# Performance work log

Hardware: AMD Instinct MI355X
Metric: run time of the kernel (lower is better)

## Reference

```python
import jax, jax.numpy as jnp
import numpy as np
import math

L_LAYERS = 2; B = 2; SEQ = 1024; D = 512; N = 16; H = 8; DH = 64; P = 32; KC = 4; DTR = 32

def _silu(x):
    return x * jax.nn.sigmoid(x)

def _rms(x, w, eps=1e-6):
    return x * jax.lax.rsqrt(jnp.mean(x * x, axis=-1, keepdims=True) + eps) * w

def _mamba(x, Win, conv_w, conv_b, Wx, Wdt, bdt, Alog, Dp, Wout):
    # x: [b,l,d]; mamba-ssm reference math with expand=1 (d_inner == d)
    b, l, d = x.shape
    xz = x @ Win                                   # [b,l,2d]
    xc, z = jnp.split(xz, 2, axis=-1)
    xp = jnp.pad(xc, ((0, 0), (KC - 1, 0), (0, 0)))  # causal depthwise conv
    xc = sum(xp[:, k:k + l, :] * conv_w[:, k] for k in range(KC)) + conv_b
    xc = _silu(xc)
    dbl = xc @ Wx                                  # [b,l,dtr+2N]
    dt = dbl[..., :DTR]
    Bc = dbl[..., DTR:DTR + N]                     # [b,l,N]
    Cc = dbl[..., DTR + N:]                        # [b,l,N]
    dt = jax.nn.softplus(dt @ Wdt + bdt)           # [b,l,d]
    A = -jnp.exp(Alog)                             # [d,N]
    dA = jnp.exp(dt[..., None] * A)                # [b,l,d,N]
    dBu = dt[..., None] * Bc[:, :, None, :] * xc[..., None]  # [b,l,d,N]
    def step(h, inp):
        dA_t, dBu_t, C_t = inp
        h = dA_t * h + dBu_t                       # [b,d,N]
        return h, jnp.einsum('bdn,bn->bd', h, C_t)
    h0 = jnp.zeros((b, d, N), x.dtype)
    _, ys = jax.lax.scan(step, h0, (dA.transpose(1, 0, 2, 3), dBu.transpose(1, 0, 2, 3), Cc.transpose(1, 0, 2)))
    y = ys.transpose(1, 0, 2) + Dp * xc
    y = y * _silu(z)
    return y @ Wout

def _enformer_attn(q, k, vv, u, vb, w):
    # q,k,vv: [b,l,h,d]; u,vb: [h,d]; w: [h,d,P]
    b, l, h, d = q.shape
    Pd = w.shape[-1]
    pos = jnp.arange(l)
    dist = pos[None, :] - pos[:, None]             # [l,l]
    pow_rate = jnp.exp(jnp.log((l + 1) / 2.0) / (Pd // 2))
    cw = pow_rate ** jnp.arange(1, Pd // 2 + 1, dtype=jnp.float32)
    ub = (jnp.abs(dist)[:, :, None].astype(jnp.float32) <= cw)
    sb = jnp.sign(dist)[:, :, None].astype(jnp.float32) * ub.astype(jnp.float32)
    basis = jnp.concatenate([ub.astype(jnp.float32), sb], axis=-1)  # [l,l,P]
    scale = 1.0 / math.sqrt(d)
    # qr_term without materializing r[h,l,l,d]: (q@w) then contract with basis
    qw = jnp.einsum('bihd,hdn->bhin', q, w)
    qr = jnp.einsum('bhin,ijn->bhij', qw, basis)
    uk = jnp.einsum('hd,bjhd->bhj', u, k)[:, :, None, :]
    vr = jnp.einsum('hn,ijn->hij', jnp.einsum('hd,hdn->hn', vb, w), basis)
    scores = jnp.einsum('bihd,bjhd->bhij', q, k) * scale + (qr + uk + vr[None]) * scale
    attn = jax.nn.softmax(scores, axis=-1)
    return jnp.einsum('bhij,bjhd->bihd', attn, vv)

def _forward(x, rms_m, W_in, b_in, m_Win, m_conv_w, m_conv_b, m_Wx, m_Wdt, m_bdt, m_Alog, m_D, m_Wout, W_out, b_out, rms_a, Wq, Wk, Wv, u, v, w_rel, Wo, b_o):
    b, l, dm = x.shape
    for i in range(L_LAYERS):
        # --- BidirectionalMamba block (tie_in_proj=True, tie_gate=False) ---
        skip = x
        xn = _rms(x, rms_m[i])
        proj = xn @ W_in[i] + b_in[i]              # [b,l,3*dm]
        xf = proj[..., :dm]
        zf = proj[..., dm:2 * dm]
        zr = proj[..., 2 * dm:]
        yf = _mamba(xf, m_Win[i, 0], m_conv_w[i, 0], m_conv_b[i, 0], m_Wx[i, 0], m_Wdt[i, 0], m_bdt[i, 0], m_Alog[i, 0], m_D[i, 0], m_Wout[i, 0])
        yr = jnp.flip(_mamba(jnp.flip(xf, axis=1), m_Win[i, 1], m_conv_w[i, 1], m_conv_b[i, 1], m_Wx[i, 1], m_Wdt[i, 1], m_bdt[i, 1], m_Alog[i, 1], m_D[i, 1], m_Wout[i, 1]), axis=1)
        y = yf * _silu(zf) + yr * _silu(zr)
        x = y @ W_out[i] + b_out[i] + skip
        # --- Enformer relative-position attention block ---
        skip = x
        xn = _rms(x, rms_a[i])
        q = (xn @ Wq[i]).reshape(b, l, H, DH)
        k = (xn @ Wk[i]).reshape(b, l, H, DH)
        vv = (xn @ Wv[i]).reshape(b, l, H, DH)
        o = _enformer_attn(q, k, vv, u[i], v[i], w_rel[i]).reshape(b, l, H * DH)
        x = skip + o @ Wo[i] + b_o[i]
    return x

def setup_inputs() -> dict:
    key = jax.random.key(0)
    ks = iter(jax.random.split(key, 48))
    def rn(shape, s=0.02):
        return jax.random.normal(next(ks), shape, dtype=jnp.float32) * s
    L = L_LAYERS
    inp = {}
    inp['x'] = jax.random.normal(next(ks), (B, SEQ, D), dtype=jnp.float32)
    inp['rms_m'] = jnp.ones((L, D), jnp.float32)
    inp['W_in'] = rn((L, D, 3 * D)); inp['b_in'] = jnp.zeros((L, 3 * D), jnp.float32)
    inp['m_Win'] = rn((L, 2, D, 2 * D))
    inp['m_conv_w'] = rn((L, 2, D, KC), 0.1); inp['m_conv_b'] = jnp.zeros((L, 2, D), jnp.float32)
    inp['m_Wx'] = rn((L, 2, D, DTR + 2 * N))
    inp['m_Wdt'] = rn((L, 2, DTR, D), 0.1); inp['m_bdt'] = rn((L, 2, D), 0.5)
    inp['m_Alog'] = jnp.tile(jnp.log(jnp.arange(1, N + 1, dtype=jnp.float32)), (L, 2, D, 1))
    inp['m_D'] = jnp.ones((L, 2, D), jnp.float32)
    inp['m_Wout'] = rn((L, 2, D, D))
    inp['W_out'] = rn((L, D, D)); inp['b_out'] = jnp.zeros((L, D), jnp.float32)
    inp['rms_a'] = jnp.ones((L, D), jnp.float32)
    inp['Wq'] = rn((L, D, H * DH)); inp['Wk'] = rn((L, D, H * DH)); inp['Wv'] = rn((L, D, H * DH))
    inp['u'] = rn((L, H, DH), 0.1); inp['v'] = rn((L, H, DH), 0.1)
    inp['w_rel'] = rn((L, H, DH, P), 0.1)
    inp['Wo'] = rn((L, H * DH, D)); inp['b_o'] = jnp.zeros((L, D), jnp.float32)
    return inp

def reference(x, rms_m, W_in, b_in, m_Win, m_conv_w, m_conv_b, m_Wx, m_Wdt, m_bdt, m_Alog, m_D, m_Wout, W_out, b_out, rms_a, Wq, Wk, Wv, u, v, w_rel, Wo, b_o):
    return _forward(x, rms_m, W_in, b_in, m_Win, m_conv_w, m_conv_b, m_Wx, m_Wdt, m_bdt, m_Alog, m_D, m_Wout, W_out, b_out, rms_a, Wq, Wk, Wv, u, v, w_rel, Wo, b_o)
```

## Files before the change

### kernel.cpp

```cpp
#include <hip/hip_runtime.h>

#define LL 2
#define BB 2
#define SEQL 1024
#define DD 512
#define NN 16
#define HH 8
#define DHH 64
#define PPB 32
#define KCC 4
#define DTRR 32

#define GBS 4
#define TC 32
#define NC (SEQL / TC)
#define NR (GBS * DD * NN)
#define BHN (BB * HH * SEQL)

#define AR_L     4325376L
#define OFF_WIN  0L
#define OFF_MWIN 786432L
#define OFF_WT2  1835008L
#define OFF_MWOUT 2490368L
#define OFF_WOUT 3014656L
#define OFF_QKV  3276800L
#define OFF_WO   4063232L

typedef __attribute__((ext_vector_type(8))) short bf16x8;
typedef __attribute__((ext_vector_type(4))) short short4v;
typedef __attribute__((ext_vector_type(4))) float f32x4;

__device__ __forceinline__ float siluf(float x) { return x / (1.f + __expf(-x)); }
__device__ __forceinline__ float softplusf(float x) { return x > 20.f ? x : log1pf(__expf(x)); }

__device__ __forceinline__ unsigned short f2bf(float x) {
  union { float f; unsigned u; } v; v.f = x;
  unsigned r = v.u + 0x7fff + ((v.u >> 16) & 1);
  return (unsigned short)(r >> 16);
}

__device__ __forceinline__ bf16x8 ld_frag(const unsigned short* p) {
  short4v a = *(const short4v*)(p);
  short4v b = *(const short4v*)(p + 4);
  bf16x8 r;
  r[0]=a[0]; r[1]=a[1]; r[2]=a[2]; r[3]=a[3];
  r[4]=b[0]; r[5]=b[1]; r[6]=b[2]; r[7]=b[3];
  return r;
}

__device__ __forceinline__ bf16x8 pack8(const float* p) {
  bf16x8 r;
  #pragma unroll
  for (int e = 0; e < 8; e++) r[e] = (short)f2bf(p[e]);
  return r;
}

struct TD { const float* src; unsigned short* dst; int ldsrc; int K; int N; int t0; };
struct TDs { TD a[24]; };

__global__ __launch_bounds__(256) void wtrans_all(TDs ds)
{
  int bid = blockIdx.x;
  int mi = 0;
  #pragma unroll 1
  for (int i = 1; i < 24; i++) if (bid >= ds.a[i].t0) mi = i;
  TD d = ds.a[mi];
  int local = bid - d.t0;
  int tilesN = d.N >> 5;
  int tn = local % tilesN, tk = local / tilesN;
  __shared__ float t[32][33];
  int tx = threadIdx.x & 31, ty = threadIdx.x >> 5;
  int n0 = tn * 32, k0 = tk * 32;
  #pragma unroll
  for (int i = 0; i < 4; i++)
    t[ty + 8 * i][tx] = d.src[(long)(k0 + ty + 8 * i) * d.ldsrc + n0 + tx];
  __syncthreads();
  #pragma unroll
  for (int i = 0; i < 4; i++)
    d.dst[(long)(n0 + ty + 8 * i) * d.K + k0 + tx] = f2bf(t[tx][ty + 8 * i]);
}

__global__ __launch_bounds__(256) void weff_kernel(
    const float* __restrict__ Wx, const float* __restrict__ Wdt,
    unsigned short* __restrict__ WTA)
{
  int lg = blockIdx.z;
  int l = lg >> 1, g = lg & 1;
  const float* wx = Wx + (long)(l * 2 + g) * DD * 64;
  const float* wd = Wdt + (long)(l * 2 + g) * DTRR * DD;
  unsigned short* wt = WTA + (long)l * AR_L + OFF_WT2 + (long)g * 327680;
  int n0 = blockIdx.x * 32, k0 = blockIdx.y * 32;
  __shared__ float wx_s[32][33];
  __shared__ float wd_s[32][33];
  int tx = threadIdx.x & 31, ty = threadIdx.x >> 5;
  #pragma unroll
  for (int i = 0; i < 4; i++) {
    wx_s[ty + 8 * i][tx] = wx[(long)(k0 + ty + 8 * i) * 64 + tx];
    wd_s[ty + 8 * i][tx] = wd[(long)(ty + 8 * i) * DD + n0 + tx];
  }
  __syncthreads();
  #pragma unroll
  for (int i = 0; i < 4; i++) {
    int nl = ty + 8 * i;
    float s = 0.f;
    #pragma unroll
    for (int r = 0; r < 32; r++) s = fmaf(wx_s[tx][r], wd_s[r][nl], s);
    wt[(long)(n0 + nl) * DD + k0 + tx] = f2bf(s);
  }
}

__global__ __launch_bounds__(256) void rmsinv_kernel(
    const float* __restrict__ x, float* __restrict__ inv)
{
  int row = blockIdx.x * 4 + (threadIdx.x >> 6);
  int lane = threadIdx.x & 63;
  const float* xr = x + (long)row * DD;
  float4 a = *(const float4*)(xr + lane * 4);
  float4 b = *(const float4*)(xr + 256 + lane * 4);
  float s = a.x*a.x + a.y*a.y + a.z*a.z + a.w*a.w + b.x*b.x + b.y*b.y + b.z*b.z + b.w*b.w;
  for (int o = 32; o; o >>= 1) s += __shfl_down(s, o);
  if (lane == 0) inv[row] = rsqrtf(s / (float)DD + 1e-6f);
}

template<int BM, int BN>
__global__ __launch_bounds__(256) void gemm_bf16_t(
    const float* __restrict__ A, const unsigned short* __restrict__ WT,
    const float* __restrict__ bias, const float* __restrict__ resid,
    const float* __restrict__ invrow, const float* __restrict__ colw,
    float* __restrict__ C,
    int M, int N, int K, int lda, int ldc,
    long aBatch, long wBatch, long biasBatch, long cBatch,
    int aflipL, int act)
{
  constexpr int FM = BM / 32;
  constexpr int FN = BN / 32;
  int g = blockIdx.z;
  A  += (long)g * aBatch;
  WT += (long)g * wBatch;
  C  += (long)g * cBatch;
  if (bias) bias += (long)g * biasBatch;
  const bool flip = (aflipL > 0) && (g == 1);

  __shared__ unsigned short A_lds[BM][72];
  __shared__ unsigned short B_lds[BN][72];
  int tid = threadIdx.x;
  int w = tid >> 6, lane = tid & 63, li = lane & 15, lg = lane >> 4;
  int bm = blockIdx.y * BM, bn = blockIdx.x * BN;
  int wm = (w & 1) * (BM / 2), wn = (w >> 1) * (BN / 2);
  f32x4 acc[FM][FN] = {};

  const int kqA = (tid & 15) * 4, r0A = tid >> 4;
  const int kqB = (tid & 7) * 8,  r0B = tid >> 3;

  for (int k0 = 0; k0 < K; k0 += 64) {
    __syncthreads();
    float4 cw4 = {1.f, 1.f, 1.f, 1.f};
    if (colw) cw4 = *(const float4*)(colw + k0 + kqA);
    #pragma unroll
    for (int i = 0; i < BM / 16; i++) {
      int m = bm + r0A + 16 * i;
      int mm = m;
      if (flip) { int bb = m / aflipL; int t = m - bb * aflipL; mm = bb * aflipL + (aflipL - 1 - t); }
      float4 av = *(const float4*)(A + (long)mm * lda + k0 + kqA);
      float sc = invrow ? invrow[mm] : 1.f;
      short4v ap = { (short)f2bf(av.x * sc * cw4.x), (short)f2bf(av.y * sc * cw4.y),
                     (short)f2bf(av.z * sc * cw4.z), (short)f2bf(av.w * sc * cw4.w) };
      *(short4v*)(&A_lds[r0A + 16 * i][kqA]) = ap;
    }
    #pragma unroll
    for (int i = 0; i < BN / 32; i++) {
      int n = bn + r0B + 32 * i;
      bf16x8 bv = *(const bf16x8*)(WT + (long)n * K + k0 + kqB);
      *(bf16x8*)(&B_lds[r0B + 32 * i][kqB]) = bv;
    }
    __syncthreads();
    #pragma unroll
    for (int ks = 0; ks < 2; ks++) {
      bf16x8 af[FM], bfr[FN];
      #pragma unroll
      for (int fm = 0; fm < FM; fm++)
        af[fm] = *(const bf16x8*)(&A_lds[wm + fm * 16 + li][ks * 32 + lg * 8]);
      #pragma unroll
      for (int fn = 0; fn < FN; fn++)
        bfr[fn] = *(const bf16x8*)(&B_lds[wn + fn * 16 + li][ks * 32 + lg * 8]);
      #pragma unroll
      for (int fm = 0; fm < FM; fm++)
        #pragma unroll
        for (int fn = 0; fn < FN; fn++)
          acc[fm][fn] = __builtin_amdgcn_mfma_f32_16x16x32_bf16(af[fm], bfr[fn], acc[fm][fn], 0, 0, 0);
    }
  }
  #pragma unroll
  for (int fm = 0; fm < FM; fm++) {
    #pragma unroll
    for (int fn = 0; fn < FN; fn++) {
      int n = bn + wn + fn * 16 + li;
      float bv = bias ? bias[n] : 0.f;
      #pragma unroll
      for (int r = 0; r < 4; r++) {
        int m = bm + wm + fm * 16 + 4 * lg + r;
        float v = acc[fm][fn][r] + bv;
        if (act == 1) v = softplusf(v);
        if (resid) v += resid[(long)m * ldc + n];
        C[(long)m * ldc + n] = v;
      }
    }
  }
}

__global__ __launch_bounds__(256) void gemm_comb(
    const float* __restrict__ yp, const float* __restrict__ proj,
    const unsigned short* __restrict__ WT,
    const float* __restrict__ bias, const float* __restrict__ resid,
    float* __restrict__ C)
{
  __shared__ unsigned short A_lds[64][72];
  __shared__ unsigned short B_lds[64][72];
  int tid = threadIdx.x;
  int w = tid >> 6, lane = tid & 63, li = lane & 15, lg = lane >> 4;
  int bm = blockIdx.y * 64, bn = blockIdx.x * 64;
  int wm = (w & 1) * 32, wn = (w >> 1) * 32;
  f32x4 acc[2][2] = {};
  const long U = (long)BB * SEQL * DD;

  const int kqA = (tid & 15) * 4, r0A = tid >> 4;
  const int kqB = (tid & 7) * 8,  r0B = tid >> 3;

  for (int k0 = 0; k0 < DD; k0 += 64) {
    __syncthreads();
    #pragma unroll
    for (int i = 0; i < 4; i++) {
      int m = bm + r0A + 16 * i;
      int t = m & (SEQL - 1), b = m >> 10;
      int mf = (b << 10) + (SEQL - 1 - t);
      float4 y0 = *(const float4*)(yp + (long)m * DD + k0 + kqA);
      float4 y1 = *(const float4*)(yp + U + (long)mf * DD + k0 + kqA);
      float4 zf = *(const float4*)(proj + (long)m * 3 * DD + DD + k0 + kqA);
      float4 zr = *(const float4*)(proj + (long)m * 3 * DD + 2 * DD + k0 + kqA);
      float4 v;
      v.x = y0.x * siluf(zf.x) + y1.x * siluf(zr.x);
      v.y = y0.y * siluf(zf.y) + y1.y * siluf(zr.y);
      v.z = y0.z * siluf(zf.z) + y1.z * siluf(zr.z);
      v.w = y0.w * siluf(zf.w) + y1.w * siluf(zr.w);
      short4v ap = { (short)f2bf(v.x), (short)f2bf(v.y), (short)f2bf(v.z), (short)f2bf(v.w) };
      *(short4v*)(&A_lds[r0A + 16 * i][kqA]) = ap;
    }
    #pragma unroll
    for (int i = 0; i < 2; i++) {
      int n = bn + r0B + 32 * i;
      bf16x8 bv = *(const bf16x8*)(WT + (long)n * DD + k0 + kqB);
      *(bf16x8*)(&B_lds[r0B + 32 * i][kqB]) = bv;
    }
    __syncthreads();
    #pragma unroll
    for (int ks = 0; ks < 2; ks++) {
      bf16x8 af[2], bfr[2];
      #pragma unroll
      for (int fm = 0; fm < 2; fm++)
        af[fm] = *(const bf16x8*)(&A_lds[wm + fm * 16 + li][ks * 32 + lg * 8]);
      #pragma unroll
      for (int fn = 0; fn < 2; fn++)
        bfr[fn] = *(const bf16x8*)(&B_lds[wn + fn * 16 + li][ks * 32 + lg * 8]);
      #pragma unroll
      for (int fm = 0; fm < 2; fm++)
        #pragma unroll
        for (int fn = 0; fn < 2; fn++)
          acc[fm][fn] = __builtin_amdgcn_mfma_f32_16x16x32_bf16(af[fm], bfr[fn], acc[fm][fn], 0, 0, 0);
    }
  }
  #pragma unroll
  for (int fm = 0; fm < 2; fm++) {
    #pragma unroll
    for (int fn = 0; fn < 2; fn++) {
      int n = bn + wn + fn * 16 + li;
      float bv = bias[n];
      #pragma unroll
      for (int r = 0; r < 4; r++) {
        int m = bm + wm + fm * 16 + 4 * lg + r;
        C[(long)m * DD + n] = acc[fm][fn][r] + bv + resid[(long)m * DD + n];
      }
    }
  }
}

__global__ __launch_bounds__(256) void gemm_attn(
    const float* __restrict__ opart, const float* __restrict__ mbuf, const float* __restrict__ lbuf,
    const unsigned short* __restrict__ WT,
    const float* __restrict__ bias, const float* __restrict__ resid,
    float* __restrict__ C)
{
  __shared__ unsigned short A_lds[64][72];
  __shared__ unsigned short B_lds[64][72];
  int tid = threadIdx.x;
  int w = tid >> 6, lane = tid & 63, li = lane & 15, lg = lane >> 4;
  int bm = blockIdx.y * 64, bn = blockIdx.x * 64;
  int wm = (w & 1) * 32, wn = (w >> 1) * 32;
  f32x4 acc[2][2] = {};

  const int kqA = (tid & 15) * 4, r0A = tid >> 4;
  const int kqB = (tid & 7) * 8,  r0B = tid >> 3;

  for (int k0 = 0; k0 < DD; k0 += 64) {
    __syncthreads();
    int h = k0 >> 6;
    #pragma unroll
    for (int i = 0; i < 4; i++) {
      int m = bm + r0A + 16 * i;
      int iseq = m & (SEQL - 1), b = m >> 10;
      long row = ((long)(b * HH + h) << 10) + iseq;
      float m0 = mbuf[row], m1 = mbuf[BHN + row];
      float l0 = lbuf[row], l1 = lbuf[BHN + row];
      float mm = fmaxf(m0, m1);
      float e0 = __expf(m0 - mm), e1 = __expf(m1 - mm);
      float inv = 1.f / (l0 * e0 + l1 * e1);
      e0 *= inv; e1 *= inv;
      float4 o0 = *(const float4*)(opart + row * 64 + kqA);
      float4 o1 = *(const float4*)(opart + ((long)BHN + row) * 64 + kqA);
      float4 v;
      v.x = o0.x * e0 + o1.x * e1;
      v.y = o0.y * e0 + o1.y * e1;
      v.z = o0.z * e0 + o1.z * e1;
      v.w = o0.w * e0 + o1.w * e1;
      short4v ap = { (short)f2bf(v.x), (short)f2bf(v.y), (short)f2bf(v.z), (short)f2bf(v.w) };
      *(short4v*)(&A_lds[r0A + 16 * i][kqA]) = ap;
    }
    #pragma unroll
    for (int i = 0; i < 2; i++) {
      int n = bn + r0B + 32 * i;
      bf16x8 bv = *(const bf16x8*)(WT + (long)n * DD + k0 + kqB);
      *(bf16x8*)(&B_lds[r0B + 32 * i][kqB]) = bv;
    }
    __syncthreads();
    #pragma unroll
    for (int ks = 0; ks < 2; ks++) {
      bf16x8 af[2], bfr[2];
      #pragma unroll
      for (int fm = 0; fm < 2; fm++)
        af[fm] = *(const bf16x8*)(&A_lds[wm + fm * 16 + li][ks * 32 + lg * 8]);
      #pragma unroll
      for (int fn = 0; fn < 2; fn++)
        bfr[fn] = *(const bf16x8*)(&B_lds[wn + fn * 16 + li][ks * 32 + lg * 8]);
      #pragma unroll
      for (int fm = 0; fm < 2; fm++)
        #pragma unroll
        for (int fn = 0; fn < 2; fn++)
          acc[fm][fn] = __builtin_amdgcn_mfma_f32_16x16x32_bf16(af[fm], bfr[fn], acc[fm][fn], 0, 0, 0);
    }
  }
  #pragma unroll
  for (int fm = 0; fm < 2; fm++) {
    #pragma unroll
    for (int fn = 0; fn < 2; fn++) {
      int n = bn + wn + fn * 16 + li;
      float bv = bias[n];
      #pragma unroll
      for (int r = 0; r < 4; r++) {
        int m = bm + wm + fm * 16 + 4 * lg + r;
        C[(long)m * DD + n] = acc[fm][fn][r] + bv + resid[(long)m * DD + n];
      }
    }
  }
}

__global__ __launch_bounds__(256) void gemm_dtbc(
    const float* __restrict__ A, const unsigned short* __restrict__ WT2,
    const float* __restrict__ bdt, float* __restrict__ dtv, float* __restrict__ bc,
    int layer)
{
  int g = blockIdx.z;
  A   += (long)g * BB * SEQL * DD;
  WT2 += (long)g * 640 * DD;
  dtv += (long)g * BB * SEQL * DD;
  bc  += (long)g * BB * SEQL * 32;
  bdt += (long)(layer * 2 + g) * DD;

  __shared__ unsigned short A_lds[64][72];
  __shared__ unsigned short B_lds[64][72];
  int tid = threadIdx.x;
  int w = tid >> 6, lane = tid & 63, li = lane & 15, lg = lane >> 4;
  int bm = blockIdx.y * 64, bn = blockIdx.x * 64;
  int wm = (w & 1) * 32, wn = (w >> 1) * 32;
  f32x4 acc[2][2] = {};

  const int kqA = (tid & 15) * 4, r0A = tid >> 4;
  const int kqB = (tid & 7) * 8,  r0B = tid >> 3;

  for (int k0 = 0; k0 < DD; k0 += 64) {
    __syncthreads();
    #pragma unroll
    for (int i = 0; i < 4; i++) {
      int m = bm + r0A + 16 * i;
      float4 av = *(const float4*)(A + (long)m * DD + k0 + kqA);
      short4v ap = { (short)f2bf(av.x), (short)f2bf(av.y), (short)f2bf(av.z), (short)f2bf(av.w) };
      *(short4v*)(&A_lds[r0A + 16 * i][kqA]) = ap;
    }
    #pragma unroll
    for (int i = 0; i < 2; i++) {
      int n = bn + r0B + 32 * i;
      bf16x8 bv = *(const bf16x8*)(WT2 + (long)n * DD + k0 + kqB);
      *(bf16x8*)(&B_lds[r0B + 32 * i][kqB]) = bv;
    }
    __syncthreads();
    #pragma unroll
    for (int ks = 0; ks < 2; ks++) {
      bf16x8 af[2], bfr[2];
      #pragma unroll
      for (int fm = 0; fm < 2; fm++)
        af[fm] = *(const bf16x8*)(&A_lds[wm + fm * 16 + li][ks * 32 + lg * 8]);
      #pragma unroll
      for (int fn = 0; fn < 2; fn++)
        bfr[fn] = *(const bf16x8*)(&B_lds[wn + fn * 16 + li][ks * 32 + lg * 8]);
      #pragma unroll
      for (int fm = 0; fm < 2; fm++)
        #pragma unroll
        for (int fn = 0; fn < 2; fn++)
          acc[fm][fn] = __builtin_amdgcn_mfma_f32_16x16x32_bf16(af[fm], bfr[fn], acc[fm][fn], 0, 0, 0);
    }
  }
  #pragma unroll
  for (int fm = 0; fm < 2; fm++) {
    #pragma unroll
    for (int fn = 0; fn < 2; fn++) {
      int n = bn + wn + fn * 16 + li;
      if (n < 512) {
        float bv = bdt[n];
        #pragma unroll
        for (int r = 0; r < 4; r++) {
          int m = bm + wm + fm * 16 + 4 * lg + r;
          dtv[(long)m * DD + n] = softplusf(acc[fm][fn][r] + bv);
        }
      } else if (n < 544) {
        #pragma unroll
        for (int r = 0; r < 4; r++) {
          int m = bm + wm + fm * 16 + 4 * lg + r;
          bc[(long)m * 32 + (n - 512)] = acc[fm][fn][r];
        }
      }
    }
  }
}

__global__ __launch_bounds__(256) void conv_silu_kernel(
    const float* __restrict__ xz, const float* __restrict__ cw, const float* __restrict__ cb,
    float* __restrict__ xc, int layer)
{
  long idx = (long)blockIdx.x * 256 + threadIdx.x;
  int c = idx % DD;
  long r = idx / DD;
  int t = r % SEQL;
  long gb = r / SEQL;
  int g = (int)(gb / BB);
  const float* w = cw + ((long)(layer * 2 + g) * DD + c) * KCC;
  float acc = cb[(long)(layer * 2 + g) * DD + c];
  const float* xp = xz + (r - t) * 2 * DD + c;
  #pragma unroll
  for (int k = 0; k < KCC; k++) {
    int tt = t - (KCC - 1) + k;
    if (tt >= 0) acc = fmaf(xp[(long)tt * 2 * DD], w[k], acc);
  }
  xc[idx] = siluf(acc);
}

__global__ __launch_bounds__(256) void scan_chunk_kernel(
    const float* __restrict__ dtv, const float* __restrict__ xc,
    const float* __restrict__ bc, const float* __restrict__ Alog,
    float* __restrict__ P, float* __restrict__ Hend, int layer)
{
  int chunk = blockIdx.x, dtile = blockIdx.y, gb = blockIdx.z;
  int g = gb / BB;
  int tid = threadIdx.x;
  int dl = tid >> 1, nh = (tid & 1) * 8;
  int d = dtile * 128 + dl;
  int t0 = chunk * TC;
  __shared__ float dtv_s[TC][128], xc_s[TC][128], BC_s[TC][32];
  {
    long base = ((long)gb * SEQL + t0) * DD + dtile * 128;
    int c4 = (tid & 31) * 4, r0 = tid >> 5;
    #pragma unroll
    for (int i = 0; i < 4; i++) {
      int tl = r0 + i * 8;
      *(float4*)&dtv_s[tl][c4] = *(const float4*)(dtv + base + (long)tl * DD + c4);
      *(float4*)&xc_s[tl][c4]  = *(const float4*)(xc + base + (long)tl * DD + c4);
    }
    long dbase = ((long)gb * SEQL + t0) * 32;
    int cc = (tid & 7) * 4, rr = tid >> 3;
    *(float4*)&BC_s[rr][cc] = *(const float4*)(bc + dbase + (long)rr * 32 + cc);
  }
  __syncthreads();
  const float* Al = Alog + ((long)((layer * 2 + g) * DD) + d) * NN + nh;
  float a[8], h[8] = {};
  #pragma unroll
  for (int n = 0; n < 8; n++) a[n] = -__expf(Al[n]);
  float sdt = 0.f;
  for (int t = 0; t < TC; t++) {
    float dt = dtv_s[t][dl];
    float dx = dt * xc_s[t][dl];
    float4 b0 = *(const float4*)&BC_s[t][nh];
    float4 b1 = *(const float4*)&BC_s[t][nh + 4];
    h[0] = fmaf(__expf(dt * a[0]), h[0], dx * b0.x);
    h[1] = fmaf(__expf(dt * a[1]), h[1], dx * b0.y);
    h[2] = fmaf(__expf(dt * a[2]), h[2], dx * b0.z);
    h[3] = fmaf(__expf(dt * a[3]), h[3], dx * b0.w);
    h[4] = fmaf(__expf(dt * a[4]), h[4], dx * b1.x);
    h[5] = fmaf(__expf(dt * a[5]), h[5], dx * b1.y);
    h[6] = fmaf(__expf(dt * a[6]), h[6], dx * b1.z);
    h[7] = fmaf(__expf(dt * a[7]), h[7], dx * b1.w);
    sdt += dt;
  }
  long o = (long)chunk * NR + ((long)(gb * DD + d)) * NN + nh;
  #pragma unroll
  for (int n = 0; n < 8; n++) {
    P[o + n] = __expf(a[n] * sdt);
    Hend[o + n] = h[n];
  }
}

__global__ __launch_bounds__(256) void scan_combine_kernel(
    const float* __restrict__ P, const float* __restrict__ Hend, float* __restrict__ Hin)
{
  int r = blockIdx.x * 256 + threadIdx.x;
  float h = 0.f;
  #pragma unroll
  for (int c = 0; c < NC; c++) {
    Hin[(long)c * NR + r] = h;
    h = fmaf(P[(long)c * NR + r], h, Hend[(long)c * NR + r]);
  }
}

__global__ __launch_bounds__(256) void scan_apply_kernel(
    const float* __restrict__ dtv, const float* __restrict__ xc, const float* __restrict__ xz,
    const float* __restrict__ bc, const float* __restrict__ Alog, const float* __restrict__ Dp,
    const float* __restrict__ Hin, float* __restrict__ ym, int layer)
{
  int chunk = blockIdx.x, dtile = blockIdx.y, gb = blockIdx.z;
  int g = gb / BB;
  int tid = threadIdx.x;
  int dl = tid >> 1, nh = (tid & 1) * 8;
  int d = dtile * 128 + dl;
  int t0 = chunk * TC;
  __shared__ float dtv_s[TC][128], xc_s[TC][128], BC_s[TC][32], y_s[TC][128];
  {
    long base = ((long)gb * SEQL + t0) * DD + dtile * 128;
    int c4 = (tid & 31) * 4, r0 = tid >> 5;
    #pragma unroll
    for (int i = 0; i < 4; i++) {
      int tl = r0 + i * 8;
      *(float4*)&dtv_s[tl][c4] = *(const float4*)(dtv + base + (long)tl * DD + c4);
      *(float4*)&xc_s[tl][c4]  = *(const float4*)(xc + base + (long)tl * DD + c4);
    }
    long dbase = ((long)gb * SEQL + t0) * 32;
    int cc = (tid & 7) * 4, rr = tid >> 3;
    *(float4*)&BC_s[rr][cc] = *(const float4*)(bc + dbase + (long)rr * 32 + cc);
  }
  __syncthreads();
  const float* Al = Alog + ((long)((layer * 2 + g) * DD) + d) * NN + nh;
  float a[8], h[8];
  #pragma unroll
  for (int n = 0; n < 8; n++) a[n] = -__expf(Al[n]);
  {
    long r = (long)chunk * NR + ((long)(gb * DD + d)) * NN + nh;
    float4 h0 = *(const float4*)(Hin + r);
    float4 h1 = *(const float4*)(Hin + r + 4);
    h[0]=h0.x; h[1]=h0.y; h[2]=h0.z; h[3]=h0.w;
    h[4]=h1.x; h[5]=h1.y; h[6]=h1.z; h[7]=h1.w;
  }
  for (int t = 0; t < TC; t++) {
    float dt = dtv_s[t][dl];
    float dx = dt * xc_s[t][dl];
    float4 b0 = *(const float4*)&BC_s[t][nh];
    float4 b1 = *(const float4*)&BC_s[t][nh + 4];
    float4 c0 = *(const float4*)&BC_s[t][16 + nh];
    float4 c1 = *(const float4*)&BC_s[t][16 + nh + 4];
    h[0] = fmaf(__expf(dt * a[0]), h[0], dx * b0.x);
    h[1] = fmaf(__expf(dt * a[1]), h[1], dx * b0.y);
    h[2] = fmaf(__expf(dt * a[2]), h[2], dx * b0.z);
    h[3] = fmaf(__expf(dt * a[3]), h[3], dx * b0.w);
    h[4] = fmaf(__expf(dt * a[4]), h[4], dx * b1.x);
    h[5] = fmaf(__expf(dt * a[5]), h[5], dx * b1.y);
    h[6] = fmaf(__expf(dt * a[6]), h[6], dx * b1.z);
    h[7] = fmaf(__expf(dt * a[7]), h[7], dx * b1.w);
    float v0 = h[0] * c0.x + h[1] * c0.y;
    float v1 = h[2] * c0.z + h[3] * c0.w;
    float v2 = h[4] * c1.x + h[5] * c1.y;
    float v3 = h[6] * c1.z + h[7] * c1.w;
    float val = (v0 + v1) + (v2 + v3);
    val += __shfl_xor(val, 1);
    if ((tid & 1) == 0) y_s[t][dl] = val;
  }
  __syncthreads();
  {
    long base = ((long)gb * SEQL + t0) * DD + dtile * 128;
    long zbase = ((long)gb * SEQL + t0) * 2 * DD + DD + dtile * 128;
    int c4 = (tid & 31) * 4, r0 = tid >> 5;
    float4 Dp4 = *(const float4*)(Dp + (long)(layer * 2 + g) * DD + dtile * 128 + c4);
    #pragma unroll
    for (int i = 0; i < 4; i++) {
      int tl = r0 + i * 8;
      float4 y4 = *(const float4*)&y_s[tl][c4];
      float4 x4 = *(const float4*)&xc_s[tl][c4];
      float4 z4 = *(const float4*)(xz + zbase + (long)tl * 2 * DD + c4);
      float4 o;
      o.x = (y4.x + Dp4.x * x4.x) * siluf(z4.x);
      o.y = (y4.y + Dp4.y * x4.y) * siluf(z4.y);
      o.z = (y4.z + Dp4.z * x4.z) * siluf(z4.z);
      o.w = (y4.w + Dp4.w * x4.w) * siluf(z4.w);
      *(float4*)(ym + base + (long)tl * DD + c4) = o;
    }
  }
}

__global__ void tab_kernel(unsigned short* __restrict__ tab)
{
  int idx = blockIdx.x * blockDim.x + threadIdx.x;
  if (idx >= 2047) return;
  int di = idx - 1023;
  int ad = di < 0 ? -di : di;
  float pr = expf(logf((SEQL + 1) * 0.5f) / 16.0f);
  int n0 = 16;
  for (int n = 15; n >= 0; n--) {
    float cw = powf(pr, (float)(n + 1));
    if ((float)ad <= cw) n0 = n;
  }
  tab[idx] = (unsigned short)(di == 0 ? 34 : (di < 0 ? n0 : 17 + n0));
}

__global__ __launch_bounds__(256) void qw_kernel(
    const float* __restrict__ q, const float* __restrict__ w_rel, float* __restrict__ S, int layer)
{
  int itile = blockIdx.x;
  int bh = blockIdx.y;
  int h = bh % HH, b = bh / HH;
  int i0 = itile * 64;
  __shared__ float q_s[64][65];
  __shared__ float w_s[64][33];
  __shared__ float qwn[64][33];
  int tid = threadIdx.x;
  {
    int r = tid >> 2, c4 = (tid & 3) * 16;
    const float* qr = q + ((long)(b * SEQL + i0 + r)) * DD + h * 64 + c4;
    #pragma unroll
    for (int e = 0; e < 4; e++) {
      float4 v = *(const float4*)(qr + e * 4);
      q_s[r][c4 + e * 4 + 0] = v.x; q_s[r][c4 + e * 4 + 1] = v.y;
      q_s[r][c4 + e * 4 + 2] = v.z; q_s[r][c4 + e * 4 + 3] = v.w;
    }
  }
  for (int idx = tid; idx < 64 * 32; idx += 256) {
    int d = idx >> 5, n = idx & 31;
    w_s[d][n] = w_rel[((long)(layer * HH + h) * DHH + d) * PPB + n];
  }
  __syncthreads();
  {
    int i = tid & 63, ngrp = tid >> 6;
    float acc[8] = {};
    #pragma unroll 8
    for (int d = 0; d < 64; d++) {
      float qv = q_s[i][d];
      #pragma unroll
      for (int e = 0; e < 8; e++) acc[e] = fmaf(qv, w_s[d][ngrp * 8 + e], acc[e]);
    }
    #pragma unroll
    for (int e = 0; e < 8; e++) qwn[i][ngrp * 8 + e] = acc[e];
  }
  __syncthreads();
  for (int idx = tid; idx < 64 * 17; idx += 256) {
    int il = idx / 17, m = idx % 17;
    float s1 = 0.f, s2 = 0.f;
    for (int n = m; n < 16; n++) { s1 += qwn[il][n]; s2 += qwn[il][16 + n]; }
    float* Sp = S + ((long)bh * SEQL + i0 + il) * 34;
    Sp[m] = s1;
    Sp[17 + m] = s2;
  }
}

__global__ __launch_bounds__(256) void vw_kernel(
    const float* __restrict__ vparam, const float* __restrict__ w_rel, float* __restrict__ VS)
{
  int layer = blockIdx.x;
  __shared__ float vws[HH][PPB];
  int tid = threadIdx.x;
  int h = tid / PPB, n = tid % PPB;
  const float* vp = vparam + (long)(layer * HH + h) * DHH;
  const float* wp = w_rel + ((long)(layer * HH + h) * DHH) * PPB + n;
  float s = 0.f;
  for (int d = 0; d < DHH; d++) s = fmaf(vp[d], wp[d * PPB], s);
  vws[h][n] = s;
  __syncthreads();
  if (tid < HH * 17) {
    int hh = tid / 17, m = tid % 17;
    float s1 = 0.f, s2 = 0.f;
    for (int nn = m; nn < 16; nn++) { s1 += vws[hh][nn]; s2 += vws[hh][16 + nn]; }
    VS[layer * 272 + hh * 34 + m] = s1;
    VS[layer * 272 + hh * 34 + 17 + m] = s2;
  }
}

__global__ __launch_bounds__(256) void uk_kernel(
    const float* __restrict__ u, const float* __restrict__ k, float* __restrict__ uk, int layer)
{
  int wid = (blockIdx.x * 256 + threadIdx.x) >> 6;
  int lane = threadIdx.x & 63;
  if (wid >= BB * HH * SEQL) return;
  int j = wid % SEQL;
  int bh = wid / SEQL;
  int h = bh % HH;
  int b = bh / HH;
  float vv = u[(long)(layer * HH + h) * DHH + lane] * k[((long)(b * SEQL + j) * HH + h) * DHH + lane];
  for (int o = 32; o; o >>= 1) vv += __shfl_down(vv, o);
  if (lane == 0) uk[(long)bh * SEQL + j] = vv;
}

__global__ __launch_bounds__(256) void attn_mfma_kernel(
    const float* __restrict__ q, const float* __restrict__ k, const float* __restrict__ vv,
    const float* __restrict__ S, const float* __restrict__ VS, const float* __restrict__ uk,
    const unsigned short* __restrict__ tab,
    float* __restrict__ opart, float* __restrict__ mbuf, float* __restrict__ lbuf)
{
  __shared__ __align__(16) char smem[39680];
  unsigned short* K_lds  = (unsigned short*)(smem);
  unsigned short* VT_lds = (unsigned short*)(smem + 8704);
  unsigned short* PT_lds = (unsigned short*)(smem + 17408);
  float* E               = (float*)(smem + 26112);
  unsigned short* tab_s  = (unsigned short*)(smem + 35328);
  float* uk_s            = (float*)(smem + 39424);
  float* O_lds           = (float*)(smem);

  int itile = blockIdx.x;
  int bh = blockIdx.y;
  int split = blockIdx.z;
  int h = bh % HH, b = bh / HH;
  int i0 = itile * 64;
  int tid = threadIdx.x;
  int w = tid >> 6;
  int lane = tid & 63;
  int li = lane & 15, lg = lane >> 4;

  for (int idx = tid; idx < 64 * 17; idx += 256) {
    int il = idx / 17, m = idx % 17;
    long srow = ((long)bh * SEQL + i0 + il) * 34;
    float c0 = S[srow + m]      + VS[h * 34 + m];
    float c1 = S[srow + 17 + m] + VS[h * 34 + 17 + m];
    E[il * 36 + m]      = c0 - c1;
    E[il * 36 + 17 + m] = c0 + c1;
    if (m == 0) E[il * 36 + 34] = c0;
  }
  for (int idx = tid; idx < 2047; idx += 256) tab_s[idx] = tab[idx];

  int iq = i0 + w * 16 + li;
  const float* qrow = q + ((long)(b * SEQL + iq)) * DD + h * 64;
  bf16x8 qf0 = pack8(qrow + 8 * lg);
  bf16x8 qf1 = pack8(qrow + 32 + 8 * lg);

  f32x4 oacc[4] = {};
  float mrun = -1e30f, lrun = 0.f;
  const int ibase = i0 + w * 16 + li;
  unsigned short* PTw = PT_lds + w * 16 * 68;
  const float* Erow = E + (w * 16 + li) * 36;

  const int jbase = split * (SEQL / 2);
  for (int jt = 0; jt < SEQL / 2; jt += 64) {
    int j0 = jbase + jt;
    __syncthreads();
    {
      int jl = tid >> 4;
      int dq = (tid & 15) * 4;
      #pragma unroll
      for (int rr = 0; rr < 4; rr++) {
        int jj = jl + rr * 16;
        long grow = ((long)(b * SEQL + j0 + jj)) * DD + h * 64 + dq;
        float4 kv = *(const float4*)(k + grow);
        short4v kp = { (short)f2bf(kv.x), (short)f2bf(kv.y), (short)f2bf(kv.z), (short)f2bf(kv.w) };
        *(short4v*)(K_lds + jj * 68 + dq) = kp;
        float4 vvv = *(const float4*)(vv + grow);
        VT_lds[(dq + 0) * 68 + jj] = f2bf(vvv.x);
        VT_lds[(dq + 1) * 68 + jj] = f2bf(vvv.y);
        VT_lds[(dq + 2) * 68 + jj] = f2bf(vvv.z);
        VT_lds[(dq + 3) * 68 + jj] = f2bf(vvv.w);
      }
      if (tid < 64) uk_s[tid] = uk[(long)bh * SEQL + j0 + tid];
    }
    __syncthreads();

    f32x4 sf[4];
    #pragma unroll
    for (int jj = 0; jj < 4; jj++) {
      f32x4 c = {};
      c = __builtin_amdgcn_mfma_f32_16x16x32_bf16(
            ld_frag(K_lds + (jj * 16 + li) * 68 + 8 * lg), qf0, c, 0, 0, 0);
      c = __builtin_amdgcn_mfma_f32_16x16x32_bf16(
            ld_frag(K_lds + (jj * 16 + li) * 68 + 32 + 8 * lg), qf1, c, 0, 0, 0);
      sf[jj] = c;
    }

    float sv[4][4];
    float tmax = -1e30f;
    #pragma unroll
    for (int jj = 0; jj < 4; jj++) {
      #pragma unroll
      for (int r = 0; r < 4; r++) {
        int jloc = jj * 16 + 4 * lg + r;
        int di = (j0 + jloc) - ibase;
        int id = tab_s[1023 + di];
        float val = (sf[jj][r] + Erow[id] + uk_s[jloc]) * 0.125f;
        sv[jj][r] = val;
        tmax = fmaxf(tmax, val);
      }
    }
    tmax = fmaxf(tmax, __shfl_xor(tmax, 16));
    tmax = fmaxf(tmax, __shfl_xor(tmax, 32));
    float mnew = fmaxf(mrun, tmax);
    float fsc = __expf(mrun - mnew);
    mrun = mnew;
    lrun *= fsc;
    #pragma unroll
    for (int df = 0; df < 4; df++) oacc[df] *= fsc;

    float psum = 0.f;
    #pragma unroll
    for (int jj = 0; jj < 4; jj++) {
      short4v pk;
      #pragma unroll
      for (int r = 0; r < 4; r++) {
        float p = __expf(sv[jj][r] - mnew);
        psum += p;
        pk[r] = (short)f2bf(p);
      }
      *(short4v*)(PTw + li * 68 + jj * 16 + 4 * lg) = pk;
    }
    psum += __shfl_xor(psum, 16);
    psum += __shfl_xor(psum, 32);
    lrun += psum;

    asm volatile("s_waitcnt lgkmcnt(0)" ::: "memory");

    bf16x8 pf0 = ld_frag(PTw + li * 68 + 8 * lg);
    bf16x8 pf1 = ld_frag(PTw + li * 68 + 32 + 8 * lg);
    #pragma unroll
    for (int df = 0; df < 4; df++) {
      f32x4 c = oacc[df];
      c = __builtin_amdgcn_mfma_f32_16x16x32_bf16(
            ld_frag(VT_lds + (df * 16 + li) * 68 + 8 * lg), pf0, c, 0, 0, 0);
      c = __builtin_amdgcn_mfma_f32_16x16x32_bf16(
            ld_frag(VT_lds + (df * 16 + li) * 68 + 32 + 8 * lg), pf1, c, 0, 0, 0);
      oacc[df] = c;
    }
  }

  __syncthreads();
  if (lg == 0) {
    long row = (long)split * BHN + (long)bh * SEQL + (i0 + w * 16 + li);
    mbuf[row] = mrun;
    lbuf[row] = lrun;
  }
  #pragma unroll
  for (int df = 0; df < 4; df++)
    *(f32x4*)(O_lds + (w * 16 + li) * 68 + df * 16 + 4 * lg) = oacc[df];
  __syncthreads();
  {
    int il = tid >> 2, c0 = (tid & 3) * 16;
    long orow = ((long)split * BHN + (long)bh * SEQL + i0 + il) * 64 + c0;
    #pragma unroll
    for (int c4 = 0; c4 < 4; c4++) {
      f32x4 o = *(const f32x4*)(O_lds + il * 68 + c0 + c4 * 4);
      *(f32x4*)(opart + orow + c4 * 4) = o;
    }
  }
}

extern "C" void kernel_launch(void* const* d_in, const int* in_sizes, int n_in,
                              void* d_out, int out_size, void* d_ws, size_t ws_size,
                              hipStream_t stream) {
  const float* x_in     = (const float*)d_in[0];
  const float* rms_m    = (const float*)d_in[1];
  const float* W_in     = (const float*)d_in[2];
  const float* b_in     = (const float*)d_in[3];
  const float* m_Win    = (const float*)d_in[4];
  const float* m_conv_w = (const float*)d_in[5];
  const float* m_conv_b = (const float*)d_in[6];
  const float* m_Wx     = (const float*)d_in[7];
  const float* m_Wdt    = (const float*)d_in[8];
  const float* m_bdt    = (const float*)d_in[9];
  const float* m_Alog   = (const float*)d_in[10];
  const float* m_Dp     = (const float*)d_in[11];
  const float* m_Wout   = (const float*)d_in[12];
  const float* W_out    = (const float*)d_in[13];
  const float* b_out    = (const float*)d_in[14];
  const float* rms_a    = (const float*)d_in[15];
  const float* Wq       = (const float*)d_in[16];
  const float* Wk       = (const float*)d_in[17];
  const float* Wv       = (const float*)d_in[18];
  const float* u_p      = (const float*)d_in[19];
  const float* v_p      = (const float*)d_in[20];
  const float* w_rel    = (const float*)d_in[21];
  const float* Wo       = (const float*)d_in[22];
  const float* b_o      = (const float*)d_in[23];
  float* out = (float*)d_out;

  float* ws = (float*)d_ws;
  const long U = (long)BB * SEQL * DD;
  float* xA    = ws;
  float* xB    = ws + 1 * U;
  float* xn    = ws + 2 * U;
  float* proj  = ws + 3 * U;
  float* xz    = ws + 6 * U;
  float* xc    = ws + 10 * U;
  float* dtv   = ws + 12 * U;
  float* ym    = ws + 14 * U;
  float* ycomb = ws + 16 * U;
  float* smallb= ws + 17 * U;
  float* bcbuf = smallb;
  float* ukbuf = smallb + 262144;
  float* Sbuf  = smallb + 278528;
  float* VSbuf = smallb + 835584;
  unsigned short* tabg = (unsigned short*)(smallb + 836880);
  float* invm  = smallb + 838928;
  float* inva  = smallb + 840976;
  unsigned short* WTA = (unsigned short*)(ws + 18 * U);
  float* yp = xz;
  float* qb = proj;
  float* kb = proj + U;
  float* vb = proj + 2 * U;
  float* Pbuf = xn;
  float* Hend = xB;
  float* Hin  = ycomb;
  float* opart = xc;
  float* mbuf  = dtv;
  float* lbuf  = dtv + 2 * BHN;

  const int M = BB * SEQL;

  tab_kernel<<<8, 256, 0, stream>>>(tabg);

  TDs td;
  int cum = 0, idx = 0;
  auto add = [&](const float* s, unsigned short* dst, int ldsrc, int K, int N) {
    td.a[idx].src = s; td.a[idx].dst = dst; td.a[idx].ldsrc = ldsrc;
    td.a[idx].K = K; td.a[idx].N = N; td.a[idx].t0 = cum;
    cum += (N / 32) * (K / 32); idx++;
  };
  for (int l = 0; l < LL; l++) {
    unsigned short* base = WTA + (long)l * AR_L;
    add(W_in   + (long)l * DD * 3 * DD,        base + OFF_WIN,            3 * DD, DD, 3 * DD);
    add(m_Win  + (long)(l * 2 + 0) * DD * 2 * DD, base + OFF_MWIN,          2 * DD, DD, 2 * DD);
    add(m_Win  + (long)(l * 2 + 1) * DD * 2 * DD, base + OFF_MWIN + 524288, 2 * DD, DD, 2 * DD);
    add(m_Wout + (long)(l * 2 + 0) * DD * DD,  base + OFF_MWOUT,          DD, DD, DD);
    add(m_Wout + (long)(l * 2 + 1) * DD * DD,  base + OFF_MWOUT + 262144, DD, DD, DD);
    add(W_out  + (long)l * DD * DD,            base + OFF_WOUT,           DD, DD, DD);
    add(Wq     + (long)l * DD * DD,            base + OFF_QKV,            DD, DD, DD);
    add(Wk     + (long)l * DD * DD,            base + OFF_QKV + 262144,   DD, DD, DD);
    add(Wv     + (long)l * DD * DD,            base + OFF_QKV + 524288,   DD, DD, DD);
    add(Wo     + (long)l * DD * DD,            base + OFF_WO,             DD, DD, DD);
    add(m_Wx   + (long)(l * 2 + 0) * DD * 64 + 32, base + OFF_WT2 + 262144,          64, DD, 32);
    add(m_Wx   + (long)(l * 2 + 1) * DD * 64 + 32, base + OFF_WT2 + 327680 + 262144, 64, DD, 32);
  }
  wtrans_all<<<cum, 256, 0, stream>>>(td);
  weff_kernel<<<dim3(16, 16, 2 * LL), 256, 0, stream>>>(m_Wx, m_Wdt, WTA);
  vw_kernel<<<LL, 256, 0, stream>>>(v_p, w_rel, VSbuf);

  for (int layer = 0; layer < LL; layer++) {
    const float* cur = (layer == 0) ? x_in : xA;
    unsigned short* base = WTA + (long)layer * AR_L;
    rmsinv_kernel<<<M / 4, 256, 0, stream>>>(cur, invm);
    gemm_bf16_t<64, 64><<<dim3(24, 32, 1), 256, 0, stream>>>(cur, base + OFF_WIN,
        b_in + layer * 3 * DD, nullptr, invm, rms_m + layer * DD, proj,
        M, 3 * DD, DD, DD, 3 * DD, 0, 0, 0, 0, 0, 0);
    gemm_bf16_t<64, 64><<<dim3(16, 32, 2), 256, 0, stream>>>(proj, base + OFF_MWIN,
        nullptr, nullptr, nullptr, nullptr, xz, M, 2 * DD, DD, 3 * DD, 2 * DD,
        0, 524288, 0, (long)BB * SEQL * 2 * DD, SEQL, 0);
    conv_silu_kernel<<<(2 * BB * SEQL * DD) / 256, 256, 0, stream>>>(xz, m_conv_w, m_conv_b, xc, layer);
    gemm_dtbc<<<dim3(9, 32, 2), 256, 0, stream>>>(xc, base + OFF_WT2, m_bdt, dtv, bcbuf, layer);
    scan_chunk_kernel<<<dim3(NC, DD / 128, GBS), 256, 0, stream>>>(
        dtv, xc, bcbuf, m_Alog, Pbuf, Hend, layer);
    scan_combine_kernel<<<NR / 256, 256, 0, stream>>>(Pbuf, Hend, Hin);
    scan_apply_kernel<<<dim3(NC, DD / 128, GBS), 256, 0, stream>>>(
        dtv, xc, xz, bcbuf, m_Alog, m_Dp, Hin, ym, layer);
    gemm_bf16_t<64, 64><<<dim3(8, 32, 2), 256, 0, stream>>>(ym, base + OFF_MWOUT,
        nullptr, nullptr, nullptr, nullptr, yp, M, DD, DD, DD, DD,
        U, 262144, 0, U, 0, 0);
    gemm_comb<<<dim3(8, 32), 256, 0, stream>>>(yp, proj, base + OFF_WOUT,
        b_out + layer * DD, cur, xB);

    rmsinv_kernel<<<M / 4, 256, 0, stream>>>(xB, inva);
    gemm_bf16_t<64, 64><<<dim3(8, 32, 3), 256, 0, stream>>>(xB, base + OFF_QKV,
        nullptr, nullptr, inva, rms_a + layer * DD, qb, M, DD, DD, DD, DD,
        0, 262144, 0, U, 0, 0);
    qw_kernel<<<dim3(16, 16), 256, 0, stream>>>(qb, w_rel, Sbuf, layer);
    uk_kernel<<<(BB * HH * SEQL) / 4, 256, 0, stream>>>(u_p, kb, ukbuf, layer);
    attn_mfma_kernel<<<dim3(SEQL / 64, BB * HH, 2), 256, 0, stream>>>(
        qb, kb, vb, Sbuf, VSbuf + layer * 272, ukbuf, tabg, opart, mbuf, lbuf);

    float* outp = (layer == LL - 1) ? out : xA;
    gemm_attn<<<dim3(8, 32), 256, 0, stream>>>(opart, mbuf, lbuf, base + OFF_WO,
        b_o + layer * DD, xB, outp);
  }
}
```

Before: 554.7 us.

## Precompute bf16 K and transposed V once; enlarge GEMM M-tiles

Replaces the per-position u·k kernel with a kvprep kernel. It computes the u·k dot products and also writes K as bf16 and V as bf16 transposed, in per-head contiguous layouts. The attention kernel then stages K and V^T into shared memory with vector bf16 copies, instead of converting fp32 and doing scattered transposed LDS writes on every tile of every block. Separately, the GEMMs switch from 64x64 to 128x64 tiles and launch half as many blocks. The costs are an extra pass writing the bf16 copies (stored in the reused ym buffer) and lower block counts for the GEMMs.

```diff
diff --git a/kernel.cpp b/kernel.cpp
--- a/kernel.cpp
+++ b/kernel.cpp
@@ -695,23 +695,55 @@
   }
 }
 
-__global__ __launch_bounds__(256) void uk_kernel(
-    const float* __restrict__ u, const float* __restrict__ k, float* __restrict__ uk, int layer)
-{
-  int wid = (blockIdx.x * 256 + threadIdx.x) >> 6;
-  int lane = threadIdx.x & 63;
-  if (wid >= BB * HH * SEQL) return;
-  int j = wid % SEQL;
-  int bh = wid / SEQL;
-  int h = bh % HH;
-  int b = bh / HH;
-  float vv = u[(long)(layer * HH + h) * DHH + lane] * k[((long)(b * SEQL + j) * HH + h) * DHH + lane];
-  for (int o = 32; o; o >>= 1) vv += __shfl_down(vv, o);
-  if (lane == 0) uk[(long)bh * SEQL + j] = vv;
+__global__ __launch_bounds__(256) void kvprep_kernel(
+    const float* __restrict__ k, const float* __restrict__ v, const float* __restrict__ u,
+    unsigned short* __restrict__ kbf, unsigned short* __restrict__ vtbf,
+    float* __restrict__ uk, int layer)
+{
+  int itile = blockIdx.x;
+  int bh = blockIdx.y;
+  int h = bh & 7, b = bh >> 3;
+  int i0 = itile * 64;
+  int tid = threadIdx.x;
+  __shared__ float vt_s[64][65];
+  int r = tid >> 2, dseg = (tid & 3) * 16;
+  const float* krow = k + ((long)(b * SEQL + i0 + r)) * DD + h * 64 + dseg;
+  const float* vrow = v + ((long)(b * SEQL + i0 + r)) * DD + h * 64 + dseg;
+  const float* urow = u + (long)(layer * HH + h) * DHH + dseg;
+  unsigned short* kb = kbf + ((long)bh * SEQL + i0 + r) * 64 + dseg;
+  float dot = 0.f;
+  #pragma unroll
+  for (int e = 0; e < 4; e++) {
+    float4 kv = *(const float4*)(krow + e * 4);
+    short4v kp = { (short)f2bf(kv.x), (short)f2bf(kv.y), (short)f2bf(kv.z), (short)f2bf(kv.w) };
+    *(short4v*)(kb + e * 4) = kp;
+    float4 uv = *(const float4*)(urow + e * 4);
+    dot += kv.x * uv.x + kv.y * uv.y + kv.z * uv.z + kv.w * uv.w;
+    float4 vv4 = *(const float4*)(vrow + e * 4);
+    vt_s[dseg + e * 4 + 0][r] = vv4.x;
+    vt_s[dseg + e * 4 + 1][r] = vv4.y;
+    vt_s[dseg + e * 4 + 2][r] = vv4.z;
+    vt_s[dseg + e * 4 + 3][r] = vv4.w;
+  }
+  dot += __shfl_xor(dot, 1);
+  dot += __shfl_xor(dot, 2);
+  if ((tid & 3) == 0) uk[(long)bh * SEQL + i0 + r] = dot;
+  __syncthreads();
+  int d = tid >> 2, jseg = (tid & 3) * 16;
+  unsigned short* vt = vtbf + ((long)bh * 64 + d) * SEQL + i0 + jseg;
+  #pragma unroll
+  for (int e = 0; e < 4; e++) {
+    short4v vp = { (short)f2bf(vt_s[d][jseg + e * 4 + 0]),
+                   (short)f2bf(vt_s[d][jseg + e * 4 + 1]),
+                   (short)f2bf(vt_s[d][jseg + e * 4 + 2]),
+                   (short)f2bf(vt_s[d][jseg + e * 4 + 3]) };
+    *(short4v*)(vt + e * 4) = vp;
+  }
 }
 
 __global__ __launch_bounds__(256) void attn_mfma_kernel(
-    const float* __restrict__ q, const float* __restrict__ k, const float* __restrict__ vv,
+    const float* __restrict__ q, const unsigned short* __restrict__ kbf,
+    const unsigned short* __restrict__ vtbf,
     const float* __restrict__ S, const float* __restrict__ VS, const float* __restrict__ uk,
     const unsigned short* __restrict__ tab,
     float* __restrict__ opart, float* __restrict__ mbuf, float* __restrict__ lbuf)
@@ -757,26 +789,19 @@
   unsigned short* PTw = PT_lds + w * 16 * 68;
   const float* Erow = E + (w * 16 + li) * 36;
 
+  const int stR = tid >> 2, stS = (tid & 3) * 16;
+
   const int jbase = split * (SEQL / 2);
   for (int jt = 0; jt < SEQL / 2; jt += 64) {
     int j0 = jbase + jt;
     __syncthreads();
     {
-      int jl = tid >> 4;
-      int dq = (tid & 15) * 4;
-      #pragma unroll
-      for (int rr = 0; rr < 4; rr++) {
-        int jj = jl + rr * 16;
-        long grow = ((long)(b * SEQL + j0 + jj)) * DD + h * 64 + dq;
-        float4 kv = *(const float4*)(k + grow);
-        short4v kp = { (short)f2bf(kv.x), (short)f2bf(kv.y), (short)f2bf(kv.z), (short)f2bf(kv.w) };
-        *(short4v*)(K_lds + jj * 68 + dq) = kp;
-        float4 vvv = *(const float4*)(vv + grow);
-        VT_lds[(dq + 0) * 68 + jj] = f2bf(vvv.x);
-        VT_lds[(dq + 1) * 68 + jj] = f2bf(vvv.y);
-        VT_lds[(dq + 2) * 68 + jj] = f2bf(vvv.z);
-        VT_lds[(dq + 3) * 68 + jj] = f2bf(vvv.w);
-      }
+      const unsigned short* ksrc = kbf + ((long)bh * SEQL + j0 + stR) * 64 + stS;
+      *(bf16x8*)(K_lds + stR * 68 + stS)     = *(const bf16x8*)(ksrc);
+      *(bf16x8*)(K_lds + stR * 68 + stS + 8) = *(const bf16x8*)(ksrc + 8);
+      const unsigned short* vsrc = vtbf + ((long)bh * 64 + stR) * SEQL + j0 + stS;
+      *(bf16x8*)(VT_lds + stR * 68 + stS)     = *(const bf16x8*)(vsrc);
+      *(bf16x8*)(VT_lds + stR * 68 + stS + 8) = *(const bf16x8*)(vsrc + 8);
       if (tid < 64) uk_s[tid] = uk[(long)bh * SEQL + j0 + tid];
     }
     __syncthreads();
@@ -926,6 +951,8 @@
   float* opart = xc;
   float* mbuf  = dtv;
   float* lbuf  = dtv + 2 * BHN;
+  unsigned short* kbf  = (unsigned short*)ym;
+  unsigned short* vtbf = kbf + (long)BHN * 64;
 
   const int M = BB * SEQL;
 
@@ -961,10 +988,10 @@
     const float* cur = (layer == 0) ? x_in : xA;
     unsigned short* base = WTA + (long)layer * AR_L;
     rmsinv_kernel<<<M / 4, 256, 0, stream>>>(cur, invm);
-    gemm_bf16_t<64, 64><<<dim3(24, 32, 1), 256, 0, stream>>>(cur, base + OFF_WIN,
+    gemm_bf16_t<128, 64><<<dim3(24, 16, 1), 256, 0, stream>>>(cur, base + OFF_WIN,
         b_in + layer * 3 * DD, nullptr, invm, rms_m + layer * DD, proj,
         M, 3 * DD, DD, DD, 3 * DD, 0, 0, 0, 0, 0, 0);
-    gemm_bf16_t<64, 64><<<dim3(16, 32, 2), 256, 0, stream>>>(proj, base + OFF_MWIN,
+    gemm_bf16_t<128, 64><<<dim3(16, 16, 2), 256, 0, stream>>>(proj, base + OFF_MWIN,
         nullptr, nullptr, nullptr, nullptr, xz, M, 2 * DD, DD, 3 * DD, 2 * DD,
         0, 524288, 0, (long)BB * SEQL * 2 * DD, SEQL, 0);
     conv_silu_kernel<<<(2 * BB * SEQL * DD) / 256, 256, 0, stream>>>(xz, m_conv_w, m_conv_b, xc, layer);
@@ -974,20 +1001,20 @@
     scan_combine_kernel<<<NR / 256, 256, 0, stream>>>(Pbuf, Hend, Hin);
     scan_apply_kernel<<<dim3(NC, DD / 128, GBS), 256, 0, stream>>>(
         dtv, xc, xz, bcbuf, m_Alog, m_Dp, Hin, ym, layer);
-    gemm_bf16_t<64, 64><<<dim3(8, 32, 2), 256, 0, stream>>>(ym, base + OFF_MWOUT,
+    gemm_bf16_t<128, 64><<<dim3(8, 16, 2), 256, 0, stream>>>(ym, base + OFF_MWOUT,
         nullptr, nullptr, nullptr, nullptr, yp, M, DD, DD, DD, DD,
         U, 262144, 0, U, 0, 0);
     gemm_comb<<<dim3(8, 32), 256, 0, stream>>>(yp, proj, base + OFF_WOUT,
         b_out + layer * DD, cur, xB);
 
     rmsinv_kernel<<<M / 4, 256, 0, stream>>>(xB, inva);
-    gemm_bf16_t<64, 64><<<dim3(8, 32, 3), 256, 0, stream>>>(xB, base + OFF_QKV,
+    gemm_bf16_t<128, 64><<<dim3(8, 16, 3), 256, 0, stream>>>(xB, base + OFF_QKV,
         nullptr, nullptr, inva, rms_a + layer * DD, qb, M, DD, DD, DD, DD,
         0, 262144, 0, U, 0, 0);
     qw_kernel<<<dim3(16, 16), 256, 0, stream>>>(qb, w_rel, Sbuf, layer);
-    uk_kernel<<<(BB * HH * SEQL) / 4, 256, 0, stream>>>(u_p, kb, ukbuf, layer);
+    kvprep_kernel<<<dim3(16, 16), 256, 0, stream>>>(kb, vb, u_p, kbf, vtbf, ukbuf, layer);
     attn_mfma_kernel<<<dim3(SEQL / 64, BB * HH, 2), 256, 0, stream>>>(
-        qb, kb, vb, Sbuf, VSbuf + layer * 272, ukbuf, tabg, opart, mbuf, lbuf);
+        qb, kbf, vtbf, Sbuf, VSbuf + layer * 272, ukbuf, tabg, opart, mbuf, lbuf);
 
     float* outp = (layer == LL - 1) ? out : xA;
     gemm_attn<<<dim3(8, 32), 256, 0, stream>>>(opart, mbuf, lbuf, base + OFF_WO,
```

After: 654.7 us. +18.0%, slower.
